# Kernel optimization log

Measured on AMD Instinct MI355X. Metric: run time of the kernel, lower is better.

Reference implementation:

```python
import jax, jax.numpy as jnp
import numpy as np

NUM_BINS = 16
BOUND = 3.0
MIN_BIN_WIDTH = 0.001
MIN_BIN_HEIGHT = 0.001
MIN_DERIVATIVE = 0.001
MIN_LAMBDA = 0.025
EPS = 1e-06


def setup_inputs() -> dict:
    key = jax.random.key(0)
    k1, k2 = jax.random.split(key)
    inputs = jax.random.normal(k1, (16384, 64), dtype=jnp.float32)
    params_unnorm = jax.random.normal(k2, (16384, 64, 4 * NUM_BINS - 1), dtype=jnp.float32)
    return {"inputs": inputs, "params_unnorm": params_unnorm}


def _calculate_knots(lengths, lower, upper):
    knots = jnp.cumsum(lengths, axis=-1) * (upper - lower) + lower
    pad = jnp.full(knots.shape[:-1] + (1,), lower, dtype=knots.dtype)
    knots = jnp.concatenate([pad, knots], axis=-1)
    knots = knots.at[..., -1].set(upper)
    lengths = jnp.diff(knots, axis=-1)
    return lengths, knots


def _spline_forward(inputs, params_unnorm):
    K = NUM_BINS
    w, h, d, lam = jnp.split(params_unnorm, [K, 2 * K, 3 * K - 1], axis=-1)
    w = jax.nn.softmax(w, axis=-1)
    h = jax.nn.softmax(h, axis=-1)
    d = jax.nn.softplus(d)
    lam = jax.nn.sigmoid(lam)

    widths = MIN_BIN_WIDTH + (1.0 - MIN_BIN_WIDTH * K) * w
    heights = MIN_BIN_HEIGHT + (1.0 - MIN_BIN_HEIGHT * K) * h
    derivatives = MIN_DERIVATIVE + d
    lambdas = (1.0 - 2.0 * MIN_LAMBDA) * lam + MIN_LAMBDA

    widths, cumwidths = _calculate_knots(widths, -BOUND, BOUND)
    heights, cumheights = _calculate_knots(heights, -BOUND, BOUND)
    # pad derivatives on both sides with 1 - min_derivative (boundary slopes == 1 after +min_derivative math in torch code semantics)
    edge = jnp.full(derivatives.shape[:-1] + (1,), 1.0 - MIN_DERIVATIVE, dtype=derivatives.dtype)
    derivatives = jnp.concatenate([edge, derivatives, edge], axis=-1)  # [..., K+1]

    # bin search: searchsorted(cumwidths + eps, x, right=True) - 1
    bin_idx = jnp.sum((cumwidths + EPS) <= inputs[..., None], axis=-1) - 1
    idx = jnp.clip(bin_idx, 0, K - 1)[..., None]

    def sel(x):
        return jnp.take_along_axis(x, idx, axis=-1)[..., 0]

    input_widths = sel(widths)
    input_heights = sel(heights)
    input_delta = input_heights / input_widths
    input_cumwidths = sel(cumwidths)
    input_cumheights = sel(cumheights)
    input_derivatives = sel(derivatives)
    input_derivatives_plus_one = sel(derivatives[..., 1:])
    input_lambdas = sel(lambdas)

    wb = jnp.sqrt(input_derivatives / input_derivatives_plus_one)
    lwa = input_lambdas
    lwb = input_lambdas * wb
    wc = (lwa * input_derivatives + (wb - lwb) * input_derivatives_plus_one) / input_delta
    ya = input_cumheights
    yb = input_heights + input_cumheights
    l1 = 1.0 - input_lambdas
    yc = (lwb * yb + l1 * ya) / (l1 + lwb)

    waya = ya
    wbyb = wb * yb
    wcyc = wc * yc
    theta = (inputs - input_cumwidths) / input_widths
    indicator = theta <= input_lambdas
    ltheta = input_lambdas - theta
    wcyctheta = wcyc * theta
    numerator = jnp.where(indicator, wcyctheta + waya * ltheta, (wcyc - wcyctheta) - wbyb * ltheta)
    wctheta = wc * theta
    denominator = jnp.where(indicator, wctheta + ltheta, (wc - wctheta) - wb * ltheta)
    outputs = numerator / denominator
    derivative_numerator = wc * jnp.where(
        indicator, input_lambdas * (yc - ya), (wb - lwb) * (yb - yc)
    ) / input_widths
    logabsdet = jnp.log(derivative_numerator) - 2.0 * jnp.log(jnp.abs(denominator))

    outside = (inputs < -BOUND) | (inputs > BOUND)
    outputs = jnp.where(outside, inputs, outputs)
    logabsdet = jnp.where(outside, 0.0, logabsdet)
    return outputs, logabsdet


def reference(inputs, params_unnorm):
    return _spline_forward(inputs, params_unnorm)
```

## Files before the change

### kernel.cpp

```cpp
#include <hip/hip_runtime.h>
#include <math.h>

#define NBINS 16
#define BOUNDV 3.0f
#define MIN_W 0.001f
#define MIN_H 0.001f
#define MIN_D 0.001f
#define MIN_L 0.025f
#define EPSV 1e-6f

#define TPB 128
#define PPE 63

__device__ __forceinline__ float softplusf(float v) {
    return fmaxf(v, 0.f) + log1pf(__expf(-fabsf(v)));
}

__global__ __launch_bounds__(TPB) void lrs_kernel(
    const float* __restrict__ x_in,
    const float* __restrict__ params,
    float* __restrict__ out,
    int n)
{
    __shared__ float lds[TPB * PPE];
    const int tid = threadIdx.x;
    const int gid = blockIdx.x * TPB + tid;

    {
        const float4* __restrict__ src =
            (const float4*)(params + (size_t)blockIdx.x * (TPB * PPE));
        float4* dst = (float4*)lds;
        const int nvec = TPB * PPE / 4;
        for (int j = tid; j < nvec; j += TPB) {
            dst[j] = src[j];
        }
    }
    __syncthreads();

    const float x = x_in[gid];
    const float* __restrict__ p = lds + tid * PPE;

    float wv[NBINS];
    float mw = -1e30f;
    #pragma unroll
    for (int i = 0; i < NBINS; ++i) { wv[i] = p[i]; mw = fmaxf(mw, wv[i]); }
    float sw = 0.f;
    #pragma unroll
    for (int i = 0; i < NBINS; ++i) { wv[i] = __expf(wv[i] - mw); sw += wv[i]; }
    const float invw = 1.f / sw;

    float cum = 0.f;
    float knp = -BOUNDV;
    int   bin = 0;
    float cw  = -BOUNDV;
    float cwn = 0.f;
    #pragma unroll
    for (int i = 0; i < NBINS; ++i) {
        cum += fmaf(0.984f, wv[i] * invw, MIN_W);
        float kn = (i == NBINS - 1) ? BOUNDV : fmaf(6.f, cum, -BOUNDV);
        bool hit = (knp + EPSV <= x);
        if (i == 0) { cwn = kn; }
        else if (hit) { bin = i; cw = knp; cwn = kn; }
        knp = kn;
    }

    float hv[NBINS];
    float mh = -1e30f;
    #pragma unroll
    for (int i = 0; i < NBINS; ++i) { hv[i] = p[16 + i]; mh = fmaxf(mh, hv[i]); }
    float sh = 0.f;
    #pragma unroll
    for (int i = 0; i < NBINS; ++i) { hv[i] = __expf(hv[i] - mh); sh += hv[i]; }
    const float invh = 1.f / sh;

    float cumh = 0.f;
    float khp = -BOUNDV;
    float ya = -BOUNDV;
    float yb = 0.f;
    #pragma unroll
    for (int i = 0; i < NBINS; ++i) {
        cumh += fmaf(0.984f, hv[i] * invh, MIN_H);
        float kh = (i == NBINS - 1) ? BOUNDV : fmaf(6.f, cumh, -BOUNDV);
        if (i == bin) { ya = khp; yb = kh; }
        khp = kh;
    }

    const float draw_lo = p[32 + bin - 1];
    const float draw_hi = p[32 + bin];
    const float d_k  = (bin == 0)         ? (1.f - MIN_D) : (MIN_D + softplusf(draw_lo));
    const float d_k1 = (bin == NBINS - 1) ? (1.f - MIN_D) : (MIN_D + softplusf(draw_hi));

    const float lraw = p[47 + bin];
    const float sig  = 1.f / (1.f + __expf(-lraw));
    const float lam  = fmaf(1.f - 2.f * MIN_L, sig, MIN_L);

    const float width  = cwn - cw;
    const float height = yb - ya;
    const float delta  = height / width;

    const float wb  = sqrtf(d_k / d_k1);
    const float lwb = lam * wb;
    const float wc  = (lam * d_k + (wb - lwb) * d_k1) / delta;
    const float l1  = 1.f - lam;
    const float yc  = (lwb * yb + l1 * ya) / (l1 + lwb);

    const float theta = (x - cw) / width;
    const bool  ind   = (theta <= lam);
    const float lt    = lam - theta;

    const float wcyc  = wc * yc;
    const float wcyct = wcyc * theta;
    const float num   = ind ? fmaf(ya, lt, wcyct)
                            : (wcyc - wcyct) - (wb * yb) * lt;
    const float wct   = wc * theta;
    const float den   = ind ? (wct + lt)
                            : (wc - wct) - wb * lt;
    float outv = num / den;

    const float dnum = wc * (ind ? lam * (yc - ya) : (wb - lwb) * (yb - yc)) / width;
    float lad = __logf(dnum) - 2.f * __logf(fabsf(den));

    const bool outside = (x < -BOUNDV) | (x > BOUNDV);
    outv = outside ? x   : outv;
    lad  = outside ? 0.f : lad;

    out[gid]     = outv;
    out[n + gid] = lad;
}

extern "C" void kernel_launch(void* const* d_in, const int* in_sizes, int n_in,
                              void* d_out, int out_size, void* d_ws, size_t ws_size,
                              hipStream_t stream) {
    const float* x      = (const float*)d_in[0];
    const float* params = (const float*)d_in[1];
    float* out          = (float*)d_out;
    const int n = in_sizes[0];
    const int blocks = n / TPB;
    lrs_kernel<<<blocks, TPB, 0, stream>>>(x, params, out, n);
}
```

Measured before the change: 380.9 us.

## Use persistent blocks with double-buffered LDS prefetch of parameter slabs

Turns the kernel into a persistent grid of 512 blocks. Each block walks over parameter slabs, prefetching the next slab into registers while it computes the current one out of LDS, with double-buffered shared memory. Divisions, sqrt and log1p are also swapped for hardware reciprocal and fast intrinsics. The risks are heavy register pressure from 16 float4 prefetch registers, lower occupancy from doubling LDS, and slightly reduced precision.

```diff
diff --git a/kernel.cpp b/kernel.cpp
--- a/kernel.cpp
+++ b/kernel.cpp
@@ -11,9 +11,25 @@
 
 #define TPB 128
 #define PPE 63
+#define SLABDW (TPB * PPE)
+#define NVEC (SLABDW / 4)
+#define TAILV (NVEC - 15 * TPB)
 
-__device__ __forceinline__ float softplusf(float v) {
-    return fmaxf(v, 0.f) + log1pf(__expf(-fabsf(v)));
+__device__ __forceinline__ float frcp(float v) { return __builtin_amdgcn_rcpf(v); }
+
+__device__ __forceinline__ void load_slab(float4* v, const float* __restrict__ params,
+                                          int s, int tid) {
+    const float4* __restrict__ src = (const float4*)(params + (size_t)s * SLABDW);
+    #pragma unroll
+    for (int k = 0; k < 15; ++k) v[k] = src[tid + k * TPB];
+    if (tid < TAILV) v[15] = src[tid + 15 * TPB];
+}
+
+__device__ __forceinline__ void store_slab(float* b, int tid, const float4* v) {
+    float4* dst = (float4*)b;
+    #pragma unroll
+    for (int k = 0; k < 15; ++k) dst[tid + k * TPB] = v[k];
+    if (tid < TAILV) dst[tid + 15 * TPB] = v[15];
 }
 
 __global__ __launch_bounds__(TPB) void lrs_kernel(
@@ -22,110 +38,127 @@
     float* __restrict__ out,
     int n)
 {
-    __shared__ float lds[TPB * PPE];
+    __shared__ __align__(16) float buf0[SLABDW];
+    __shared__ __align__(16) float buf1[SLABDW];
     const int tid = threadIdx.x;
-    const int gid = blockIdx.x * TPB + tid;
+    const int nslab = n / TPB;
+    const int g = gridDim.x;
 
-    {
-        const float4* __restrict__ src =
-            (const float4*)(params + (size_t)blockIdx.x * (TPB * PPE));
-        float4* dst = (float4*)lds;
-        const int nvec = TPB * PPE / 4;
-        for (int j = tid; j < nvec; j += TPB) {
-            dst[j] = src[j];
-        }
-    }
+    int s = blockIdx.x;
+    if (s >= nslab) return;
+
+    float4 v[16];
+    load_slab(v, params, s, tid);
+    float xc = x_in[(size_t)s * TPB + tid];
+    store_slab(buf0, tid, v);
     __syncthreads();
 
-    const float x = x_in[gid];
-    const float* __restrict__ p = lds + tid * PPE;
+    float* cur = buf0;
+    float* nxt = buf1;
 
-    float wv[NBINS];
-    float mw = -1e30f;
-    #pragma unroll
-    for (int i = 0; i < NBINS; ++i) { wv[i] = p[i]; mw = fmaxf(mw, wv[i]); }
-    float sw = 0.f;
-    #pragma unroll
-    for (int i = 0; i < NBINS; ++i) { wv[i] = __expf(wv[i] - mw); sw += wv[i]; }
-    const float invw = 1.f / sw;
+    for (; s < nslab; s += g) {
+        const int sn = s + g;
+        const bool hn = (sn < nslab);
+        float xn = 0.f;
+        if (hn) {
+            load_slab(v, params, sn, tid);
+            xn = x_in[(size_t)sn * TPB + tid];
+        }
 
-    float cum = 0.f;
-    float knp = -BOUNDV;
-    int   bin = 0;
-    float cw  = -BOUNDV;
-    float cwn = 0.f;
-    #pragma unroll
-    for (int i = 0; i < NBINS; ++i) {
-        cum += fmaf(0.984f, wv[i] * invw, MIN_W);
-        float kn = (i == NBINS - 1) ? BOUNDV : fmaf(6.f, cum, -BOUNDV);
-        bool hit = (knp + EPSV <= x);
-        if (i == 0) { cwn = kn; }
-        else if (hit) { bin = i; cw = knp; cwn = kn; }
-        knp = kn;
+        const float* p = cur + tid * PPE;
+        const float x = xc;
+
+        float wv[NBINS];
+        float mw = -1e30f;
+        #pragma unroll
+        for (int i = 0; i < NBINS; ++i) { wv[i] = p[i]; mw = fmaxf(mw, wv[i]); }
+        float sw = 0.f;
+        #pragma unroll
+        for (int i = 0; i < NBINS; ++i) { wv[i] = __expf(wv[i] - mw); sw += wv[i]; }
+        const float invw = frcp(sw);
+
+        float cum = 0.f, knp = -BOUNDV, cw = -BOUNDV, cwn = 0.f;
+        int bin = 0;
+        #pragma unroll
+        for (int i = 0; i < NBINS; ++i) {
+            cum += fmaf(0.984f, wv[i] * invw, MIN_W);
+            float kn = (i == NBINS - 1) ? BOUNDV : fmaf(6.f, cum, -BOUNDV);
+            bool hit = (knp + EPSV <= x);
+            if (i == 0) { cwn = kn; }
+            else if (hit) { bin = i; cw = knp; cwn = kn; }
+            knp = kn;
+        }
+
+        const float draw_lo = p[31 + bin];
+        const float draw_hi = p[32 + bin];
+        const float lraw    = p[47 + bin];
+
+        float hv[NBINS];
+        float mh = -1e30f;
+        #pragma unroll
+        for (int i = 0; i < NBINS; ++i) { hv[i] = p[16 + i]; mh = fmaxf(mh, hv[i]); }
+        float sh = 0.f;
+        #pragma unroll
+        for (int i = 0; i < NBINS; ++i) { hv[i] = __expf(hv[i] - mh); sh += hv[i]; }
+        const float invh = frcp(sh);
+
+        float cumh = 0.f, khp = -BOUNDV, ya = -BOUNDV, yb = 0.f;
+        #pragma unroll
+        for (int i = 0; i < NBINS; ++i) {
+            cumh += fmaf(0.984f, hv[i] * invh, MIN_H);
+            float kh = (i == NBINS - 1) ? BOUNDV : fmaf(6.f, cumh, -BOUNDV);
+            if (i == bin) { ya = khp; yb = kh; }
+            khp = kh;
+        }
+
+        const float sp_lo = fmaxf(draw_lo, 0.f) + __logf(1.f + __expf(-fabsf(draw_lo)));
+        const float sp_hi = fmaxf(draw_hi, 0.f) + __logf(1.f + __expf(-fabsf(draw_hi)));
+        const float d_k  = (bin == 0)         ? (1.f - MIN_D) : (MIN_D + sp_lo);
+        const float d_k1 = (bin == NBINS - 1) ? (1.f - MIN_D) : (MIN_D + sp_hi);
+
+        const float sig = frcp(1.f + __expf(-lraw));
+        const float lam = fmaf(1.f - 2.f * MIN_L, sig, MIN_L);
+
+        const float width  = cwn - cw;
+        const float height = yb - ya;
+        const float inv_w  = frcp(width);
+        const float inv_dl = width * frcp(height);
+
+        const float wb  = __builtin_amdgcn_sqrtf(d_k * frcp(d_k1));
+        const float lwb = lam * wb;
+        const float wc  = (lam * d_k + (wb - lwb) * d_k1) * inv_dl;
+        const float l1  = 1.f - lam;
+        const float yc  = (lwb * yb + l1 * ya) * frcp(l1 + lwb);
+
+        const float theta = (x - cw) * inv_w;
+        const bool  ind   = (theta <= lam);
+        const float lt    = lam - theta;
+
+        const float wcyc  = wc * yc;
+        const float wcyct = wcyc * theta;
+        const float num   = ind ? fmaf(ya, lt, wcyct)
+                                : (wcyc - wcyct) - (wb * yb) * lt;
+        const float wct   = wc * theta;
+        const float den   = ind ? (wct + lt)
+                                : (wc - wct) - wb * lt;
+        float outv = num * frcp(den);
+
+        const float dnum = wc * (ind ? lam * (yc - ya) : (wb - lwb) * (yb - yc)) * inv_w;
+        float lad = __logf(dnum) - 2.f * __logf(fabsf(den));
+
+        const bool outside = (x < -BOUNDV) | (x > BOUNDV);
+        outv = outside ? x   : outv;
+        lad  = outside ? 0.f : lad;
+
+        const size_t gid = (size_t)s * TPB + tid;
+        out[gid]     = outv;
+        out[n + gid] = lad;
+
+        if (hn) store_slab(nxt, tid, v);
+        __syncthreads();
+        float* t = cur; cur = nxt; nxt = t;
+        xc = xn;
     }
-
-    float hv[NBINS];
-    float mh = -1e30f;
-    #pragma unroll
-    for (int i = 0; i < NBINS; ++i) { hv[i] = p[16 + i]; mh = fmaxf(mh, hv[i]); }
-    float sh = 0.f;
-    #pragma unroll
-    for (int i = 0; i < NBINS; ++i) { hv[i] = __expf(hv[i] - mh); sh += hv[i]; }
-    const float invh = 1.f / sh;
-
-    float cumh = 0.f;
-    float khp = -BOUNDV;
-    float ya = -BOUNDV;
-    float yb = 0.f;
-    #pragma unroll
-    for (int i = 0; i < NBINS; ++i) {
-        cumh += fmaf(0.984f, hv[i] * invh, MIN_H);
-        float kh = (i == NBINS - 1) ? BOUNDV : fmaf(6.f, cumh, -BOUNDV);
-        if (i == bin) { ya = khp; yb = kh; }
-        khp = kh;
-    }
-
-    const float draw_lo = p[32 + bin - 1];
-    const float draw_hi = p[32 + bin];
-    const float d_k  = (bin == 0)         ? (1.f - MIN_D) : (MIN_D + softplusf(draw_lo));
-    const float d_k1 = (bin == NBINS - 1) ? (1.f - MIN_D) : (MIN_D + softplusf(draw_hi));
-
-    const float lraw = p[47 + bin];
-    const float sig  = 1.f / (1.f + __expf(-lraw));
-    const float lam  = fmaf(1.f - 2.f * MIN_L, sig, MIN_L);
-
-    const float width  = cwn - cw;
-    const float height = yb - ya;
-    const float delta  = height / width;
-
-    const float wb  = sqrtf(d_k / d_k1);
-    const float lwb = lam * wb;
-    const float wc  = (lam * d_k + (wb - lwb) * d_k1) / delta;
-    const float l1  = 1.f - lam;
-    const float yc  = (lwb * yb + l1 * ya) / (l1 + lwb);
-
-    const float theta = (x - cw) / width;
-    const bool  ind   = (theta <= lam);
-    const float lt    = lam - theta;
-
-    const float wcyc  = wc * yc;
-    const float wcyct = wcyc * theta;
-    const float num   = ind ? fmaf(ya, lt, wcyct)
-                            : (wcyc - wcyct) - (wb * yb) * lt;
-    const float wct   = wc * theta;
-    const float den   = ind ? (wct + lt)
-                            : (wc - wct) - wb * lt;
-    float outv = num / den;
-
-    const float dnum = wc * (ind ? lam * (yc - ya) : (wb - lwb) * (yb - yc)) / width;
-    float lad = __logf(dnum) - 2.f * __logf(fabsf(den));
-
-    const bool outside = (x < -BOUNDV) | (x > BOUNDV);
-    outv = outside ? x   : outv;
-    lad  = outside ? 0.f : lad;
-
-    out[gid]     = outv;
-    out[n + gid] = lad;
 }
 
 extern "C" void kernel_launch(void* const* d_in, const int* in_sizes, int n_in,
@@ -135,6 +168,6 @@
     const float* params = (const float*)d_in[1];
     float* out          = (float*)d_out;
     const int n = in_sizes[0];
-    const int blocks = n / TPB;
+    const int blocks = 512;
     lrs_kernel<<<blocks, TPB, 0, stream>>>(x, params, out, n);
 }
```

Result: slower. 400.5 us (+5.1%).
